# Optimization experiments

Measured on AMD Instinct MI355X. Metric: run time of the kernel, lower is better.

Reference implementation:

```python
import jax, jax.numpy as jnp
from jax import lax
import numpy as np

EPS_BN = 1e-5


def _convT(x, w, b, s, p):
    # PyTorch ConvTranspose2d(w: (Cin,Cout,k,k)) as gradient-of-conv.
    k = w.shape[2]
    wf = jnp.flip(w, (2, 3)).transpose(1, 0, 2, 3)  # (Cout,Cin,k,k)
    y = lax.conv_general_dilated(x, wf, (1, 1), [(k - 1 - p, k - 1 - p)] * 2,
                                 lhs_dilation=(s, s),
                                 dimension_numbers=('NCHW', 'OIHW', 'NCHW'))
    return y + b[None, :, None, None]


def _bn_relu(x, g, b):
    # BatchNorm2d in training mode (batch stats, biased var) + ReLU
    m = x.mean((0, 2, 3), keepdims=True)
    v = x.var((0, 2, 3), keepdims=True)
    return jax.nn.relu(g[None, :, None, None] * (x - m) * lax.rsqrt(v + EPS_BN) + b[None, :, None, None])


def _sn(w, u):
    # One power iteration (detached, as in the torch SpectralNorm impl), sigma through live w.
    wm = w.reshape(w.shape[0], -1)
    wd = lax.stop_gradient(wm)
    v = wd.T @ u
    v = v / (jnp.linalg.norm(v) + 1e-12)
    un = wd @ v
    un = un / (jnp.linalg.norm(un) + 1e-12)
    sigma = un @ (wm @ v)
    return w / sigma


def _self_attn(x, wf, bf, wg, bg, wh, bh, gamma):
    # Faithful math of Self_Attn, but without materializing the (b,C,N^2,N^2) repeat.
    b_, C, f, _ = x.shape
    N = f * f
    k = C // 8
    fx = (jnp.einsum('bchw,oc->bohw', x, wf) + bf[None, :, None, None]).reshape(b_, k, N, f, f)
    gx = (jnp.einsum('bchw,oc->bohw', x, wg) + bg[None, :, None, None]).reshape(b_, k, N, f, f)
    hx = (jnp.einsum('bchw,oc->bohw', x, wh) + bh[None, :, None, None]).reshape(b_, C, N)
    # attn_dist[b,i,a,c] = sum_k f_view[b,k,i,c,a] * g_view[b,k,i,a,c]  (f spatially transposed)
    logits = jnp.einsum('bkica,bkiac->biac', fx, gx).reshape(b_, N, N)
    attn = jax.nn.softmax(logits, axis=-1)  # (b, N, N)
    out = jnp.einsum('bcj,bij->bci', hx, attn).reshape(b_, C, f, f)
    return gamma[0] * out + x, attn[:, None]


def setup_inputs() -> dict:
    key = jax.random.key(0)
    ks = iter(jax.random.split(key, 64))

    def rn(shape, s=0.02):
        return jax.random.normal(next(ks), shape, jnp.float32) * s

    def uvec(n):
        u = jax.random.normal(next(ks), (n,), jnp.float32)
        return u / jnp.linalg.norm(u)

    B, Z = 4, 100
    d = {'z': jax.random.normal(next(ks), (B, Z), jnp.float32)}
    d.update(w1=rn((Z, 512, 4, 4)), b1=jnp.zeros(512), u1=uvec(Z), g1=jnp.ones(512), be1=jnp.zeros(512))
    d.update(w2=rn((512, 256, 4, 4)), b2=jnp.zeros(256), u2=uvec(512), g2=jnp.ones(256), be2=jnp.zeros(256))
    d.update(w3=rn((256, 128, 4, 4)), b3=jnp.zeros(128), u3=uvec(256), g3=jnp.ones(128), be3=jnp.zeros(128))
    d.update(w4=rn((128, 64, 4, 4)), b4=jnp.zeros(64), u4=uvec(128), g4=jnp.ones(64), be4=jnp.zeros(64))
    d.update(wl=rn((64, 3, 4, 4)), bl=jnp.zeros(3))
    d.update(wf1=rn((4096, 128)), bf1=jnp.zeros(4096), wg1=rn((4096, 128)), bg1=jnp.zeros(4096),
             wh1=rn((128, 128)), bh1=jnp.zeros(128), gamma1=jnp.full((1,), 0.5, jnp.float32))
    d.update(wf2=rn((8192, 64)), bf2=jnp.zeros(8192), wg2=rn((8192, 64)), bg2=jnp.zeros(8192),
             wh2=rn((64, 64)), bh2=jnp.zeros(64), gamma2=jnp.full((1,), 0.5, jnp.float32))
    return d


def reference(z, w1, b1, u1, g1, be1, w2, b2, u2, g2, be2, w3, b3, u3, g3, be3,
              w4, b4, u4, g4, be4, wl, bl,
              wf1, bf1, wg1, bg1, wh1, bh1, gamma1,
              wf2, bf2, wg2, bg2, wh2, bh2, gamma2):
    x = z[:, :, None, None]                                   # (B,100,1,1)
    x = _bn_relu(_convT(x, _sn(w1, u1), b1, 1, 0), g1, be1)   # (B,512,4,4)
    x = _bn_relu(_convT(x, _sn(w2, u2), b2, 2, 1), g2, be2)   # (B,256,8,8)
    x = _bn_relu(_convT(x, _sn(w3, u3), b3, 2, 1), g3, be3)   # (B,128,16,16)
    x, p1 = _self_attn(x, wf1, bf1, wg1, bg1, wh1, bh1, gamma1)
    x = _bn_relu(_convT(x, _sn(w4, u4), b4, 2, 1), g4, be4)   # (B,64,32,32)
    x, p2 = _self_attn(x, wf2, bf2, wg2, bg2, wh2, bh2, gamma2)
    out = jnp.tanh(_convT(x, wl, bl, 2, 1))                   # (B,3,64,64)
    return out, p1, p2
```

## Files before the change

kernel.cpp:

```cpp
#include <hip/hip_runtime.h>
#include <math.h>

#define DEV __device__ __forceinline__
typedef unsigned short ushort;
typedef __attribute__((ext_vector_type(8))) short bf16x8;
typedef __attribute__((ext_vector_type(4))) float f32x4;

constexpr int ACC   = 0;
constexpr int VR1   = 16;
constexpr int VR2   = VR1 + 8192;
constexpr int VR3   = VR2 + 4096;
constexpr int VR4   = VR3 + 2048;
constexpr int WS_Y1  = 16384;
constexpr int WS_Y2  = WS_Y1 + 32768;
constexpr int WS_Y3  = WS_Y2 + 65536;
constexpr int WS_BF3 = WS_Y3 + 131072;
constexpr int WS_H1T = WS_BF3 + 131072;
constexpr int WS_X3B = WS_H1T + 131072;
constexpr int WS_Y4  = WS_X3B + 131072;
constexpr int WS_BF4 = WS_Y4 + 262144;
constexpr int WS_H2T = WS_BF4 + 262144;
constexpr int WS_X4B = WS_H2T + 262144;
constexpr int WS_WB  = WS_X4B + 262144;
constexpr int WS_PART= WS_WB + 1048576;
constexpr int WS_WT2 = WS_PART + 1048576;
constexpr int WS_WT3 = WS_WT2 + 2097152;
constexpr int WS_WT4 = WS_WT3 + 524288;
constexpr int WS_WTL = WS_WT4 + 131072;

constexpr int O_P1 = 49152;
constexpr int O_P2 = O_P1 + 262144;

DEV ushort f2bf(float v){
  unsigned b = __float_as_uint(v);
  return (ushort)((b + 0x7fffu + ((b >> 16) & 1u)) >> 16);
}
DEV float wave_sum(float v){
  #pragma unroll
  for (int o = 32; o; o >>= 1) v += __shfl_xor(v, o, 64);
  return v;
}
DEV float wave_max(float v){
  #pragma unroll
  for (int o = 32; o; o >>= 1) v = fmaxf(v, __shfl_xor(v, o, 64));
  return v;
}
template<int T>
DEV float block_sum(float v, float* sm){
  v = wave_sum(v);
  if (T == 64) return v;
  __syncthreads();
  if ((threadIdx.x & 63) == 0) sm[threadIdx.x >> 6] = v;
  __syncthreads();
  float r = 0.f;
  #pragma unroll
  for (int i = 0; i < T/64; ++i) r += sm[i];
  return r;
}
template<int T>
DEV float block_max(float v, float* sm){
  v = wave_max(v);
  if (T == 64) return v;
  __syncthreads();
  if ((threadIdx.x & 63) == 0) sm[threadIdx.x >> 6] = v;
  __syncthreads();
  float r = -INFINITY;
  #pragma unroll
  for (int i = 0; i < T/64; ++i) r = fmaxf(r, sm[i]);
  return r;
}

DEV float inv_sigma(const float* __restrict__ ws, int wi){
  float d1 = sqrtf(ws[ACC + wi]) + 1e-12f;
  float s2 = ws[ACC + 4 + wi] / (d1 * d1);
  float sig = s2 / (sqrtf(s2) + 1e-12f);
  return 1.0f / sig;
}

__global__ void zero_vr_k(float* ws){
  int tid = blockIdx.x * 256 + threadIdx.x;
  ws[VR1 + tid] = 0.f;
  if (blockIdx.x == 0 && threadIdx.x < 8) ws[ACC + threadIdx.x] = 0.f;
}

__global__ void sn1_k(const float* __restrict__ w1, const float* __restrict__ w2,
                      const float* __restrict__ w3, const float* __restrict__ w4,
                      const float* __restrict__ u1, const float* __restrict__ u2,
                      const float* __restrict__ u3, const float* __restrict__ u4,
                      float* __restrict__ ws){
  int gid = blockIdx.x * 256 + threadIdx.x;
  int col_g = gid % 15360;
  int rchunk = gid / 15360;
  const float* W; const float* U; int rows, cols, col, voff;
  if (col_g < 8192)       { W=w1; U=u1; rows=100; cols=8192; col=col_g;        voff=VR1; }
  else if (col_g < 12288) { W=w2; U=u2; rows=512; cols=4096; col=col_g-8192;   voff=VR2; }
  else if (col_g < 14336) { W=w3; U=u3; rows=256; cols=2048; col=col_g-12288;  voff=VR3; }
  else                    { W=w4; U=u4; rows=128; cols=1024; col=col_g-14336;  voff=VR4; }
  int rc = rows >> 2;
  int r0 = rchunk * rc, r1 = r0 + rc;
  float a0=0.f, a1=0.f, a2=0.f, a3=0.f;
  int i = r0;
  for (; i + 3 < r1; i += 4){
    a0 = fmaf(W[(i  )*cols + col], U[i  ], a0);
    a1 = fmaf(W[(i+1)*cols + col], U[i+1], a1);
    a2 = fmaf(W[(i+2)*cols + col], U[i+2], a2);
    a3 = fmaf(W[(i+3)*cols + col], U[i+3], a3);
  }
  for (; i < r1; ++i) a0 = fmaf(W[i*cols + col], U[i], a0);
  atomicAdd(&ws[voff + col], (a0+a1)+(a2+a3));
}

__global__ void s1red_k(float* __restrict__ ws){
  int gid = blockIdx.x * 256 + threadIdx.x;
  int wi = gid < 8192 ? 0 : gid < 12288 ? 1 : gid < 14336 ? 2 : 3;
  float v = ws[VR1 + gid];
  float sq = wave_sum(v * v);
  if ((threadIdx.x & 63) == 0) atomicAdd(&ws[ACC + wi], sq);
}

__global__ void sn2_k(const float* __restrict__ w1, const float* __restrict__ w2,
                      const float* __restrict__ w3, const float* __restrict__ w4,
                      float* __restrict__ ws){
  int wave = (blockIdx.x * 256 + threadIdx.x) >> 6;
  int lane = threadIdx.x & 63;
  if (wave >= 996) return;
  const float* W; int row, cols, wi, voff;
  if (wave < 100)      { W=w1; row=wave;     cols=8192; wi=0; voff=VR1; }
  else if (wave < 612) { W=w2; row=wave-100; cols=4096; wi=1; voff=VR2; }
  else if (wave < 868) { W=w3; row=wave-612; cols=2048; wi=2; voff=VR3; }
  else                 { W=w4; row=wave-868; cols=1024; wi=3; voff=VR4; }
  const float* Wr = W + (size_t)row * cols;
  const float* Vr = ws + voff;
  float p0=0.f, p1=0.f, p2=0.f, p3=0.f;
  for (int j = lane; j < cols; j += 256){
    p0 = fmaf(Wr[j      ], Vr[j      ], p0);
    p1 = fmaf(Wr[j +  64], Vr[j +  64], p1);
    p2 = fmaf(Wr[j + 128], Vr[j + 128], p2);
    p3 = fmaf(Wr[j + 192], Vr[j + 192], p3);
  }
  float t = wave_sum((p0+p1)+(p2+p3));
  if (lane == 0) atomicAdd(&ws[ACC + 4 + wi], t * t);
}

__global__ void wtrans_k(const float* __restrict__ w2, const float* __restrict__ w3,
                         const float* __restrict__ w4, const float* __restrict__ wl,
                         const float* __restrict__ ws,
                         float* __restrict__ wt2, float* __restrict__ wt3,
                         float* __restrict__ wt4, float* __restrict__ wtl){
  int t = blockIdx.x * 256 + threadIdx.x;
  const float* src; float* dst; int CI, CO, loc; float inv;
  if (t < 2097152)      { src=w2; dst=wt2; CI=512; CO=256; loc=t;         inv=inv_sigma(ws,1); }
  else if (t < 2621440) { src=w3; dst=wt3; CI=256; CO=128; loc=t-2097152; inv=inv_sigma(ws,2); }
  else if (t < 2752512) { src=w4; dst=wt4; CI=128; CO=64;  loc=t-2621440; inv=inv_sigma(ws,3); }
  else                  { src=wl; dst=wtl; CI=64;  CO=3;   loc=t-2752512; inv=1.f; }
  int e  = loc & 3;
  int q  = loc >> 2;
  int co = q % CO;
  int ci = (q / CO) % CI;
  int p  = q / (CO * CI);
  int kh = (1 - (p >> 1)) + 2 * (e >> 1);
  int kw = (1 - (p & 1))  + 2 * (e & 1);
  dst[loc] = src[(ci*CO + co)*16 + kh*4 + kw] * inv;
}

__global__ void cvt_w_k(const float* __restrict__ a0, const float* __restrict__ a1,
                        const float* __restrict__ a2, const float* __restrict__ a3,
                        ushort* __restrict__ dst){
  int tid = blockIdx.x * 256 + threadIdx.x;
  int seg = tid >> 19;
  int off = tid & 524287;
  const float* s = seg == 0 ? a0 : seg == 1 ? a1 : seg == 2 ? a2 : a3;
  dst[tid] = f2bf(s[off]);
}

__global__ void conv1_k(const float* __restrict__ z, const float* __restrict__ w,
                        const float* __restrict__ bias, const float* __restrict__ ws,
                        float* __restrict__ y){
  int tid = blockIdx.x * 256 + threadIdx.x;
  int s  = tid & 15;
  int co = (tid >> 4) & 511;
  int b  = tid >> 13;
  float inv = inv_sigma(ws, 0);
  const float* zb = z + b*100;
  const float* wp = w + co*16 + s;
  float a0=0.f, a1=0.f, a2=0.f, a3=0.f;
  for (int ci = 0; ci < 100; ci += 4){
    a0 = fmaf(zb[ci  ], wp[(ci  )*8192], a0);
    a1 = fmaf(zb[ci+1], wp[(ci+1)*8192], a1);
    a2 = fmaf(zb[ci+2], wp[(ci+2)*8192], a2);
    a3 = fmaf(zb[ci+3], wp[(ci+3)*8192], a3);
  }
  y[tid] = ((a0+a1)+(a2+a3)) * inv + bias[co];
}

template<int CI, int CO, int IH>
__global__ __launch_bounds__(256) void convt_par_k(const float* __restrict__ x,
                                                   const float* __restrict__ wt,
                                                   float* __restrict__ partial){
  constexpr int OH   = 2 * IH;
  constexpr int TPJ  = 4 * IH * IH;
  constexpr int CIS  = CI / 4;
  constexpr int OUTS = 4 * CO * OH * OH;
  int tid = blockIdx.x * 256 + threadIdx.x;
  int within = tid % TPJ;
  int job    = tid / TPJ;
  int co = job % CO;
  int p  = (job / CO) & 3;
  int sc = job / (CO * 4);
  co = __builtin_amdgcn_readfirstlane(co);
  p  = __builtin_amdgcn_readfirstlane(p);
  sc = __builtin_amdgcn_readfirstlane(sc);
  int b  = within / (IH * IH);
  int rc = within % (IH * IH);
  int r = rc / IH, c = rc % IH;
  int po = p >> 1, pw = p & 1;
  int ih0 = r + po, ih1 = ih0 - 1;
  int iw0 = c + pw, iw1 = iw0 - 1;
  bool vh0 = ih0 < IH, vh1 = ih1 >= 0;
  bool vw0 = iw0 < IH, vw1 = iw1 >= 0;
  int jh0 = vh0 ? ih0 : 0, jh1 = vh1 ? ih1 : 0;
  int jw0 = vw0 ? iw0 : 0, jw1 = vw1 ? iw1 : 0;
  int o00 = jh0*IH + jw0, o01 = jh0*IH + jw1;
  int o10 = jh1*IH + jw0, o11 = jh1*IH + jw1;
  const float* xb = x + (b*CI + sc*CIS) * IH * IH;
  const float* wp = wt + (size_t)((p*CI + sc*CIS)*CO + co) * 4;
  float a00=0.f, a01=0.f, a10=0.f, a11=0.f;
  #pragma unroll 4
  for (int ci = 0; ci < CIS; ++ci){
    f32x4 wv = *(const f32x4*)(wp + (size_t)ci*CO*4);
    const float* xp = xb + ci*IH*IH;
    a00 = fmaf(xp[o00], wv[0], a00);
    a01 = fmaf(xp[o01], wv[1], a01);
    a10 = fmaf(xp[o10], wv[2], a10);
    a11 = fmaf(xp[o11], wv[3], a11);
  }
  float res = (vh0 && vw0 ? a00 : 0.f) + (vh0 && vw1 ? a01 : 0.f)
            + (vh1 && vw0 ? a10 : 0.f) + (vh1 && vw1 ? a11 : 0.f);
  int oh = 2*r + po, ow = 2*c + pw;
  partial[(size_t)sc*OUTS + ((b*CO + co)*OH + oh)*OH + ow] = res;
}

__global__ void tanh_comb_k(const float* __restrict__ partial,
                            const float* __restrict__ bl, float* __restrict__ out){
  int tid = blockIdx.x * 256 + threadIdx.x;
  int co = (tid >> 12) % 3;
  float a = partial[tid] + partial[49152 + tid] + partial[2*49152 + tid]
          + partial[3*49152 + tid] + bl[co];
  out[tid] = tanhf(a);
}

template<int C, int HW, int EPT, int THREADS>
__global__ void bn_relu_k(float* __restrict__ y, const float* __restrict__ g,
                          const float* __restrict__ be){
  __shared__ float sm[8];
  int c = blockIdx.x;
  int t = threadIdx.x;
  constexpr int N = 4 * HW;
  float v[EPT];
  #pragma unroll
  for (int k = 0; k < EPT; ++k){
    int e = t + k * THREADS;
    int b = e / HW, hw = e % HW;
    v[k] = y[(b*C + c)*HW + hw];
  }
  float s = 0.f;
  #pragma unroll
  for (int k = 0; k < EPT; ++k) s += v[k];
  s = block_sum<THREADS>(s, sm);
  float m = s / (float)N;
  float q = 0.f;
  #pragma unroll
  for (int k = 0; k < EPT; ++k){ float d = v[k] - m; q = fmaf(d, d, q); }
  q = block_sum<THREADS>(q, sm);
  float rstd = rsqrtf(q / (float)N + 1e-5f);
  float gg = g[c] * rstd, bb = be[c];
  #pragma unroll
  for (int k = 0; k < EPT; ++k){
    int e = t + k * THREADS;
    int b = e / HW, hw = e % HW;
    y[(b*C + c)*HW + hw] = fmaxf(fmaf(v[k] - m, gg, bb), 0.f);
  }
}

template<int C, int HW, int EPT, int THREADS>
__global__ void bn_relu_sum_k(const float* __restrict__ partial,
                              const float* __restrict__ bias,
                              const float* __restrict__ g, const float* __restrict__ be,
                              float* __restrict__ y){
  __shared__ float sm[8];
  constexpr int OUTS = 4 * C * HW;
  int c = blockIdx.x;
  int t = threadIdx.x;
  constexpr int N = 4 * HW;
  float cb = bias[c];
  float v[EPT];
  #pragma unroll
  for (int k = 0; k < EPT; ++k){
    int e = t + k * THREADS;
    int b = e / HW, hw = e % HW;
    int idx = (b*C + c)*HW + hw;
    v[k] = partial[idx] + partial[OUTS + idx] + partial[2*OUTS + idx]
         + partial[3*OUTS + idx] + cb;
  }
  float s = 0.f;
  #pragma unroll
  for (int k = 0; k < EPT; ++k) s += v[k];
  s = block_sum<THREADS>(s, sm);
  float m = s / (float)N;
  float q = 0.f;
  #pragma unroll
  for (int k = 0; k < EPT; ++k){ float d = v[k] - m; q = fmaf(d, d, q); }
  q = block_sum<THREADS>(q, sm);
  float rstd = rsqrtf(q / (float)N + 1e-5f);
  float gg = g[c] * rstd, bb = be[c];
  #pragma unroll
  for (int k = 0; k < EPT; ++k){
    int e = t + k * THREADS;
    int b = e / HW, hw = e % HW;
    y[(b*C + c)*HW + hw] = fmaxf(fmaf(v[k] - m, gg, bb), 0.f);
  }
}

template<int C, int F>
__global__ void prep_attn_k(const float* __restrict__ x, const float* __restrict__ wh,
                            const float* __restrict__ bh,
                            ushort* __restrict__ xs, ushort* __restrict__ xts,
                            ushort* __restrict__ hb){
  constexpr int N = F * F;
  constexpr int G1 = (4 * C * N) / 256;
  int blk = blockIdx.x;
  if (blk < G1){
    int tid = blk * 256 + threadIdx.x;
    int c = tid % C;
    int s = (tid / C) % N;
    int b = tid / (C * N);
    xs[tid]  = f2bf(x[(b*C + c)*N + s]);
    int ts = (s % F) * F + s / F;
    xts[tid] = f2bf(x[(b*C + c)*N + ts]);
  } else {
    int tid = (blk - G1) * 256 + threadIdx.x;
    int j  = tid % N;
    int cc = (tid / N) % C;
    int b  = tid / (N*C);
    float a = bh[cc];
    for (int ch = 0; ch < C; ++ch)
      a = fmaf(wh[cc*C + ch], x[(b*C + ch)*N + j], a);
    hb[tid] = f2bf(a);
  }
}

template<int C, int N, int K, int JPB>
__global__ __launch_bounds__(256) void logits_mfma_res_k(
    const ushort* __restrict__ xs, const ushort* __restrict__ xts,
    const ushort* __restrict__ wfb, const ushort* __restrict__ wgb,
    const float* __restrict__ bfp, const float* __restrict__ bgp,
    float* __restrict__ out){
  constexpr int NF  = C / 32;
  constexpr int NIG = N / 64;
  constexpr int NJC = (N / 16) / JPB;
  int w = threadIdx.x >> 6, l = threadIdx.x & 63;
  int lr = l & 15, lg = l >> 4;
  int blk = blockIdx.x;
  int jc = blk % NJC;
  int ib = (blk / NJC) % NIG;
  int b  = blk / (NJC * NIG);
  int i0 = ib * 64 + w * 16;
  int j0 = jc * (JPB * 16);

  bf16x8 af[K][NF], ag[K][NF];
  f32x4 bfv[K], bgv[K];
  #pragma unroll
  for (int kk = 0; kk < K; ++kk){
    #pragma unroll
    for (int f = 0; f < NF; ++f){
      int ro = (kk*N + i0 + lr)*C + f*32 + lg*8;
      af[kk][f] = *(const bf16x8*)(wfb + ro);
      ag[kk][f] = *(const bf16x8*)(wgb + ro);
    }
    bfv[kk] = *(const f32x4*)(bfp + kk*N + i0 + lg*4);
    bgv[kk] = *(const f32x4*)(bgp + kk*N + i0 + lg*4);
  }
  const ushort* xsp  = xs  + (b*N + j0 + lr)*C + lg*8;
  const ushort* xtsp = xts + (b*N + j0 + lr)*C + lg*8;
  float* op = out + (size_t)(b*N + i0 + lg*4)*N + j0 + lr;
  for (int it = 0; it < JPB; ++it){
    bf16x8 bs[NF], bt[NF];
    #pragma unroll
    for (int f = 0; f < NF; ++f){
      bs[f] = *(const bf16x8*)(xsp  + it*16*C + f*32);
      bt[f] = *(const bf16x8*)(xtsp + it*16*C + f*32);
    }
    f32x4 acc = {0.f, 0.f, 0.f, 0.f};
    #pragma unroll
    for (int kk = 0; kk < K; ++kk){
      f32x4 F = bfv[kk], G = bgv[kk];
      #pragma unroll
      for (int f = 0; f < NF; ++f){
        F = __builtin_amdgcn_mfma_f32_16x16x32_bf16(af[kk][f], bt[f], F, 0, 0, 0);
        G = __builtin_amdgcn_mfma_f32_16x16x32_bf16(ag[kk][f], bs[f], G, 0, 0, 0);
      }
      #pragma unroll
      for (int r = 0; r < 4; ++r) acc[r] = fmaf(F[r], G[r], acc[r]);
    }
    #pragma unroll
    for (int r = 0; r < 4; ++r) op[(size_t)r*N + it*16] = acc[r];
  }
}

template<int C, int N, int K, int JPB>
__global__ __launch_bounds__(256) void logits_mfma_split_k(
    const ushort* __restrict__ xs, const ushort* __restrict__ xts,
    const ushort* __restrict__ wfb, const ushort* __restrict__ wgb,
    const float* __restrict__ bfp, const float* __restrict__ bgp,
    float* __restrict__ out){
  constexpr int NF  = C / 32;
  constexpr int KW  = K / 4;
  constexpr int NJC = (N / 16) / JPB;
  __shared__ float red[3][320];
  int w = threadIdx.x >> 6, l = threadIdx.x & 63;
  int lr = l & 15, lg = l >> 4;
  int blk = blockIdx.x;
  int jc = blk % NJC;
  int ig = (blk / NJC) % (N / 16);
  int b  = blk / (NJC * (N / 16));
  int i0 = ig * 16;
  int j0 = jc * (JPB * 16);
  int k0 = w * KW;

  bf16x8 af[KW][NF], ag[KW][NF];
  f32x4 bfv[KW], bgv[KW];
  #pragma unroll
  for (int kk = 0; kk < KW; ++kk){
    #pragma unroll
    for (int f = 0; f < NF; ++f){
      int ro = ((k0 + kk)*N + i0 + lr)*C + f*32 + lg*8;
      af[kk][f] = *(const bf16x8*)(wfb + ro);
      ag[kk][f] = *(const bf16x8*)(wgb + ro);
    }
    bfv[kk] = *(const f32x4*)(bfp + (k0 + kk)*N + i0 + lg*4);
    bgv[kk] = *(const f32x4*)(bgp + (k0 + kk)*N + i0 + lg*4);
  }
  const ushort* xsp  = xs  + (b*N + j0 + lr)*C + lg*8;
  const ushort* xtsp = xts + (b*N + j0 + lr)*C + lg*8;
  float* op = out + (size_t)(b*N + i0 + lg*4)*N + j0 + lr;
  for (int it = 0; it < JPB; ++it){
    bf16x8 bs[NF], bt[NF];
    #pragma unroll
    for (int f = 0; f < NF; ++f){
      bs[f] = *(const bf16x8*)(xsp  + it*16*C + f*32);
      bt[f] = *(const bf16x8*)(xtsp + it*16*C + f*32);
    }
    f32x4 acc = {0.f, 0.f, 0.f, 0.f};
    #pragma unroll
    for (int kk = 0; kk < KW; ++kk){
      f32x4 F = bfv[kk], G = bgv[kk];
      #pragma unroll
      for (int f = 0; f < NF; ++f){
        F = __builtin_amdgcn_mfma_f32_16x16x32_bf16(af[kk][f], bt[f], F, 0, 0, 0);
        G = __builtin_amdgcn_mfma_f32_16x16x32_bf16(ag[kk][f], bs[f], G, 0, 0, 0);
      }
      #pragma unroll
      for (int r = 0; r < 4; ++r) acc[r] = fmaf(F[r], G[r], acc[r]);
    }
    if (w > 0){
      #pragma unroll
      for (int r = 0; r < 4; ++r) red[w-1][l*5 + r] = acc[r];
    }
    __syncthreads();
    if (w == 0){
      #pragma unroll
      for (int ww = 0; ww < 3; ++ww)
        #pragma unroll
        for (int r = 0; r < 4; ++r) acc[r] += red[ww][l*5 + r];
      #pragma unroll
      for (int r = 0; r < 4; ++r) op[(size_t)r*N + it*16] = acc[r];
    }
    __syncthreads();
  }
}

template<int LEN, int EPT>
__global__ void softmax_k(float* __restrict__ p, ushort* __restrict__ pb){
  __shared__ float sm[8];
  int row = blockIdx.x;
  int t = threadIdx.x;
  float v[EPT];
  #pragma unroll
  for (int k = 0; k < EPT; ++k) v[k] = p[row*LEN + t + k*256];
  float m = -INFINITY;
  #pragma unroll
  for (int k = 0; k < EPT; ++k) m = fmaxf(m, v[k]);
  m = block_max<256>(m, sm);
  float s = 0.f;
  #pragma unroll
  for (int k = 0; k < EPT; ++k){ v[k] = expf(v[k] - m); s += v[k]; }
  s = block_sum<256>(s, sm);
  #pragma unroll
  for (int k = 0; k < EPT; ++k){
    float r = v[k] / s;
    p[row*LEN + t + k*256]  = r;
    pb[row*LEN + t + k*256] = f2bf(r);
  }
}

template<int C, int N, int KS>
__global__ __launch_bounds__(256) void attnout_mfma_k(
    const ushort* __restrict__ pb, const ushort* __restrict__ hb,
    float* __restrict__ partial){
  constexpr int NIT = N / 16;
  constexpr int NCT = C / 16;
  constexpr int KC  = N / KS;
  constexpr int NKF = KC / 32;
  constexpr int SZ  = 4 * C * N;
  int w = threadIdx.x >> 6, l = threadIdx.x & 63;
  int lr = l & 15, lg = l >> 4;
  int wid = blockIdx.x * 4 + w;
  int ks  = wid % KS;
  int cct = (wid / KS) % NCT;
  int it  = (wid / (KS * NCT)) % NIT;
  int b   = wid / (KS * NCT * NIT);
  int koff = ks * KC;

  const ushort* pp = pb + (size_t)(b*N + it*16 + lr)*N + koff + lg*8;
  bf16x8 bfr[NKF];
  #pragma unroll
  for (int f = 0; f < NKF; ++f) bfr[f] = *(const bf16x8*)(pp + f*32);
  const ushort* hp = hb + (size_t)(b*C + cct*16 + lr)*N + koff + lg*8;
  f32x4 acc = {0.f, 0.f, 0.f, 0.f};
  #pragma unroll
  for (int f = 0; f < NKF; ++f){
    bf16x8 afr = *(const bf16x8*)(hp + f*32);
    acc = __builtin_amdgcn_mfma_f32_16x16x32_bf16(afr, bfr[f], acc, 0, 0, 0);
  }
  float* op = partial + (size_t)ks*SZ + ((size_t)(b*C + cct*16 + lg*4)*N + it*16 + lr);
  #pragma unroll
  for (int r = 0; r < 4; ++r) op[(size_t)r*N] = acc[r];
}

template<int C, int N, int KS>
__global__ void attnout_fin_k(const float* __restrict__ partial,
                              const float* __restrict__ x,
                              const float* __restrict__ gamma,
                              float* __restrict__ xo){
  constexpr int SZ = 4 * C * N;
  int tid = blockIdx.x * 256 + threadIdx.x;
  float s = 0.f;
  #pragma unroll
  for (int ks = 0; ks < KS; ++ks) s += partial[(size_t)ks*SZ + tid];
  xo[tid] = fmaf(gamma[0], s, x[tid]);
}

extern "C" void kernel_launch(void* const* d_in, const int* in_sizes, int n_in,
                              void* d_out, int out_size, void* d_ws, size_t ws_size,
                              hipStream_t stream){
  const float* z   = (const float*)d_in[0];
  const float* w1  = (const float*)d_in[1];  const float* b1  = (const float*)d_in[2];
  const float* u1  = (const float*)d_in[3];  const float* g1  = (const float*)d_in[4];
  const float* be1 = (const float*)d_in[5];
  const float* w2  = (const float*)d_in[6];  const float* b2  = (const float*)d_in[7];
  const float* u2  = (const float*)d_in[8];  const float* g2  = (const float*)d_in[9];
  const float* be2 = (const float*)d_in[10];
  const float* w3  = (const float*)d_in[11]; const float* b3  = (const float*)d_in[12];
  const float* u3  = (const float*)d_in[13]; const float* g3  = (const float*)d_in[14];
  const float* be3 = (const float*)d_in[15];
  const float* w4  = (const float*)d_in[16]; const float* b4  = (const float*)d_in[17];
  const float* u4  = (const float*)d_in[18]; const float* g4  = (const float*)d_in[19];
  const float* be4 = (const float*)d_in[20];
  const float* wl  = (const float*)d_in[21]; const float* bl  = (const float*)d_in[22];
  const float* wf1 = (const float*)d_in[23]; const float* bf1 = (const float*)d_in[24];
  const float* wg1 = (const float*)d_in[25]; const float* bg1 = (const float*)d_in[26];
  const float* wh1 = (const float*)d_in[27]; const float* bh1 = (const float*)d_in[28];
  const float* gamma1 = (const float*)d_in[29];
  const float* wf2 = (const float*)d_in[30]; const float* bf2 = (const float*)d_in[31];
  const float* wg2 = (const float*)d_in[32]; const float* bg2 = (const float*)d_in[33];
  const float* wh2 = (const float*)d_in[34]; const float* bh2 = (const float*)d_in[35];
  const float* gamma2 = (const float*)d_in[36];

  float* ws  = (float*)d_ws;
  float* out = (float*)d_out;

  ushort* wb    = (ushort*)(ws + WS_WB);
  ushort* wf1b  = wb;
  ushort* wg1b  = wb + 524288;
  ushort* wf2b  = wb + 2*524288;
  ushort* wg2b  = wb + 3*524288;
  ushort* xs3   = (ushort*)(ws + WS_BF3);
  ushort* xts3  = xs3 + 131072;
  ushort* xs4   = (ushort*)(ws + WS_BF4);
  ushort* xts4  = xs4 + 262144;
  ushort* hb1   = (ushort*)(ws + WS_H1T);
  ushort* hb2   = (ushort*)(ws + WS_H2T);
  ushort* pbuf  = (ushort*)(ws + WS_WT2);
  float*  part  = ws + WS_PART;

  zero_vr_k<<<60, 256, 0, stream>>>(ws);
  sn1_k<<<240, 256, 0, stream>>>(w1, w2, w3, w4, u1, u2, u3, u4, ws);
  s1red_k<<<60, 256, 0, stream>>>(ws);
  sn2_k<<<249, 256, 0, stream>>>(w1, w2, w3, w4, ws);
  wtrans_k<<<10764, 256, 0, stream>>>(w2, w3, w4, wl, ws,
                                      ws + WS_WT2, ws + WS_WT3, ws + WS_WT4, ws + WS_WTL);
  cvt_w_k<<<8192, 256, 0, stream>>>(wf1, wg1, wf2, wg2, wb);

  conv1_k<<<128, 256, 0, stream>>>(z, w1, b1, ws, ws + WS_Y1);
  bn_relu_k<512, 16, 1, 64><<<512, 64, 0, stream>>>(ws + WS_Y1, g1, be1);

  convt_par_k<512, 256, 4><<<1024, 256, 0, stream>>>(ws + WS_Y1, ws + WS_WT2, part);
  bn_relu_sum_k<256, 64, 1, 256><<<256, 256, 0, stream>>>(part, b2, g2, be2, ws + WS_Y2);

  convt_par_k<256, 128, 8><<<2048, 256, 0, stream>>>(ws + WS_Y2, ws + WS_WT3, part);
  bn_relu_sum_k<128, 256, 4, 256><<<128, 256, 0, stream>>>(part, b3, g3, be3, ws + WS_Y3);

  prep_attn_k<128, 16><<<1024, 256, 0, stream>>>(ws + WS_Y3, wh1, bh1, xs3, xts3, hb1);
  logits_mfma_split_k<128, 256, 16, 4><<<256, 256, 0, stream>>>(
      xs3, xts3, wf1b, wg1b, bf1, bg1, out + O_P1);
  softmax_k<256, 1><<<1024, 256, 0, stream>>>(out + O_P1, pbuf);
  attnout_mfma_k<128, 256, 1><<<128, 256, 0, stream>>>(pbuf, hb1, part);
  attnout_fin_k<128, 256, 1><<<512, 256, 0, stream>>>(part, ws + WS_Y3, gamma1,
                                                      ws + WS_X3B);

  convt_par_k<128, 64, 16><<<4096, 256, 0, stream>>>(ws + WS_X3B, ws + WS_WT4, part);
  bn_relu_sum_k<64, 1024, 16, 256><<<64, 256, 0, stream>>>(part, b4, g4, be4, ws + WS_Y4);

  prep_attn_k<64, 32><<<2048, 256, 0, stream>>>(ws + WS_Y4, wh2, bh2, xs4, xts4, hb2);
  logits_mfma_res_k<64, 1024, 8, 8><<<512, 256, 0, stream>>>(
      xs4, xts4, wf2b, wg2b, bf2, bg2, out + O_P2);
  softmax_k<1024, 4><<<4096, 256, 0, stream>>>(out + O_P2, pbuf);
  attnout_mfma_k<64, 1024, 4><<<1024, 256, 0, stream>>>(pbuf, hb2, part);
  attnout_fin_k<64, 1024, 4><<<1024, 256, 0, stream>>>(part, ws + WS_Y4, gamma2,
                                                       ws + WS_X4B);

  convt_par_k<64, 3, 32><<<768, 256, 0, stream>>>(ws + WS_X4B, ws + WS_WTL, part);
  tanh_comb_k<<<192, 256, 0, stream>>>(part, bl, out);
}
```

Measured before the change: 373.3 us.

## Fuse weight prep kernels, vectorize stores, widen BN and attention-output splits

Merges the weight transpose and bf16 conversion into one launch. Each thread now reads 16 contiguous taps and writes four f32x4 vectors, and the conversion uses 4-wide loads and stores. It also unrolls the h-projection with four accumulators and raises the first attention-output split from 1 to 2. The layer-4 BN kernel moves to 1024 threads per channel, which is why the shared reduction buffer grows to 16 entries. These changes target launch overhead and uncoalesced scalar memory traffic, at the cost of more code paths and a dependence on the larger reduction buffer.

```diff
diff --git a/kernel.cpp b/kernel.cpp
--- a/kernel.cpp
+++ b/kernel.cpp
@@ -5,6 +5,7 @@
 typedef unsigned short ushort;
 typedef __attribute__((ext_vector_type(8))) short bf16x8;
 typedef __attribute__((ext_vector_type(4))) float f32x4;
+typedef __attribute__((ext_vector_type(4))) ushort us4;
 
 constexpr int ACC   = 0;
 constexpr int VR1   = 16;
@@ -142,35 +143,51 @@
   if (lane == 0) atomicAdd(&ws[ACC + 4 + wi], t * t);
 }
 
-__global__ void wtrans_k(const float* __restrict__ w2, const float* __restrict__ w3,
-                         const float* __restrict__ w4, const float* __restrict__ wl,
-                         const float* __restrict__ ws,
-                         float* __restrict__ wt2, float* __restrict__ wt3,
-                         float* __restrict__ wt4, float* __restrict__ wtl){
-  int t = blockIdx.x * 256 + threadIdx.x;
-  const float* src; float* dst; int CI, CO, loc; float inv;
-  if (t < 2097152)      { src=w2; dst=wt2; CI=512; CO=256; loc=t;         inv=inv_sigma(ws,1); }
-  else if (t < 2621440) { src=w3; dst=wt3; CI=256; CO=128; loc=t-2097152; inv=inv_sigma(ws,2); }
-  else if (t < 2752512) { src=w4; dst=wt4; CI=128; CO=64;  loc=t-2621440; inv=inv_sigma(ws,3); }
-  else                  { src=wl; dst=wtl; CI=64;  CO=3;   loc=t-2752512; inv=1.f; }
-  int e  = loc & 3;
-  int q  = loc >> 2;
-  int co = q % CO;
-  int ci = (q / CO) % CI;
-  int p  = q / (CO * CI);
-  int kh = (1 - (p >> 1)) + 2 * (e >> 1);
-  int kw = (1 - (p & 1))  + 2 * (e & 1);
-  dst[loc] = src[(ci*CO + co)*16 + kh*4 + kw] * inv;
-}
-
-__global__ void cvt_w_k(const float* __restrict__ a0, const float* __restrict__ a1,
-                        const float* __restrict__ a2, const float* __restrict__ a3,
-                        ushort* __restrict__ dst){
-  int tid = blockIdx.x * 256 + threadIdx.x;
-  int seg = tid >> 19;
-  int off = tid & 524287;
-  const float* s = seg == 0 ? a0 : seg == 1 ? a1 : seg == 2 ? a2 : a3;
-  dst[tid] = f2bf(s[off]);
+__global__ void wprep_k(const float* __restrict__ w2, const float* __restrict__ w3,
+                        const float* __restrict__ w4, const float* __restrict__ wl,
+                        const float* __restrict__ ws,
+                        float* __restrict__ wt2, float* __restrict__ wt3,
+                        float* __restrict__ wt4, float* __restrict__ wtl,
+                        const float* __restrict__ wf1, const float* __restrict__ wg1,
+                        const float* __restrict__ wf2, const float* __restrict__ wg2,
+                        ushort* __restrict__ wbdst){
+  int blk = blockIdx.x;
+  if (blk < 673){
+    int t = blk * 256 + threadIdx.x;
+    if (t >= 172224) return;
+    const float* src; float* dst; int CI, CO, loc; float inv;
+    if (t < 131072)      { src=w2; dst=wt2; CI=512; CO=256; loc=t;        inv=inv_sigma(ws,1); }
+    else if (t < 163840) { src=w3; dst=wt3; CI=256; CO=128; loc=t-131072; inv=inv_sigma(ws,2); }
+    else if (t < 172032) { src=w4; dst=wt4; CI=128; CO=64;  loc=t-163840; inv=inv_sigma(ws,3); }
+    else                 { src=wl; dst=wtl; CI=64;  CO=3;   loc=t-172032; inv=1.f; }
+    int co = loc % CO, ci = loc / CO;
+    float wv[16];
+    const float* sp = src + (size_t)(ci*CO + co) * 16;
+    #pragma unroll
+    for (int k = 0; k < 16; ++k) wv[k] = sp[k] * inv;
+    #pragma unroll
+    for (int p = 0; p < 4; ++p){
+      int po = p >> 1, pw = p & 1;
+      f32x4 o;
+      #pragma unroll
+      for (int e = 0; e < 4; ++e){
+        int kh = (1 - po) + 2 * (e >> 1);
+        int kw = (1 - pw) + 2 * (e & 1);
+        o[e] = wv[kh*4 + kw];
+      }
+      *(f32x4*)(dst + (size_t)((p*CI + ci)*CO + co) * 4) = o;
+    }
+  } else {
+    int tid = (blk - 673) * 256 + threadIdx.x;
+    int seg = tid >> 17;
+    int off = (tid & 131071) * 4;
+    const float* s = seg == 0 ? wf1 : seg == 1 ? wg1 : seg == 2 ? wf2 : wg2;
+    f32x4 v = *(const f32x4*)(s + off);
+    us4 o;
+    #pragma unroll
+    for (int k = 0; k < 4; ++k) o[k] = f2bf(v[k]);
+    *(us4*)(wbdst + (size_t)seg*524288 + off) = o;
+  }
 }
 
 __global__ void conv1_k(const float* __restrict__ z, const float* __restrict__ w,
@@ -252,7 +269,7 @@
 template<int C, int HW, int EPT, int THREADS>
 __global__ void bn_relu_k(float* __restrict__ y, const float* __restrict__ g,
                           const float* __restrict__ be){
-  __shared__ float sm[8];
+  __shared__ float sm[16];
   int c = blockIdx.x;
   int t = threadIdx.x;
   constexpr int N = 4 * HW;
@@ -287,7 +304,7 @@
                               const float* __restrict__ bias,
                               const float* __restrict__ g, const float* __restrict__ be,
                               float* __restrict__ y){
-  __shared__ float sm[8];
+  __shared__ float sm[16];
   constexpr int OUTS = 4 * C * HW;
   int c = blockIdx.x;
   int t = threadIdx.x;
@@ -342,10 +359,17 @@
     int j  = tid % N;
     int cc = (tid / N) % C;
     int b  = tid / (N*C);
-    float a = bh[cc];
-    for (int ch = 0; ch < C; ++ch)
-      a = fmaf(wh[cc*C + ch], x[(b*C + ch)*N + j], a);
-    hb[tid] = f2bf(a);
+    const float* whp = wh + cc*C;
+    const float* xp  = x + (size_t)b*C*N + j;
+    float a0 = bh[cc], a1 = 0.f, a2 = 0.f, a3 = 0.f;
+    #pragma unroll 4
+    for (int ch = 0; ch < C; ch += 4){
+      a0 = fmaf(whp[ch  ], xp[(size_t)(ch  )*N], a0);
+      a1 = fmaf(whp[ch+1], xp[(size_t)(ch+1)*N], a1);
+      a2 = fmaf(whp[ch+2], xp[(size_t)(ch+2)*N], a2);
+      a3 = fmaf(whp[ch+3], xp[(size_t)(ch+3)*N], a3);
+    }
+    hb[tid] = f2bf((a0+a1)+(a2+a3));
   }
 }
 
@@ -481,7 +505,7 @@
 
 template<int LEN, int EPT>
 __global__ void softmax_k(float* __restrict__ p, ushort* __restrict__ pb){
-  __shared__ float sm[8];
+  __shared__ float sm[16];
   int row = blockIdx.x;
   int t = threadIdx.x;
   float v[EPT];
@@ -597,9 +621,9 @@
   sn1_k<<<240, 256, 0, stream>>>(w1, w2, w3, w4, u1, u2, u3, u4, ws);
   s1red_k<<<60, 256, 0, stream>>>(ws);
   sn2_k<<<249, 256, 0, stream>>>(w1, w2, w3, w4, ws);
-  wtrans_k<<<10764, 256, 0, stream>>>(w2, w3, w4, wl, ws,
-                                      ws + WS_WT2, ws + WS_WT3, ws + WS_WT4, ws + WS_WTL);
-  cvt_w_k<<<8192, 256, 0, stream>>>(wf1, wg1, wf2, wg2, wb);
+  wprep_k<<<2721, 256, 0, stream>>>(w2, w3, w4, wl, ws,
+                                    ws + WS_WT2, ws + WS_WT3, ws + WS_WT4, ws + WS_WTL,
+                                    wf1, wg1, wf2, wg2, wb);
 
   conv1_k<<<128, 256, 0, stream>>>(z, w1, b1, ws, ws + WS_Y1);
   bn_relu_k<512, 16, 1, 64><<<512, 64, 0, stream>>>(ws + WS_Y1, g1, be1);
@@ -614,12 +638,12 @@
   logits_mfma_split_k<128, 256, 16, 4><<<256, 256, 0, stream>>>(
       xs3, xts3, wf1b, wg1b, bf1, bg1, out + O_P1);
   softmax_k<256, 1><<<1024, 256, 0, stream>>>(out + O_P1, pbuf);
-  attnout_mfma_k<128, 256, 1><<<128, 256, 0, stream>>>(pbuf, hb1, part);
-  attnout_fin_k<128, 256, 1><<<512, 256, 0, stream>>>(part, ws + WS_Y3, gamma1,
+  attnout_mfma_k<128, 256, 2><<<256, 256, 0, stream>>>(pbuf, hb1, part);
+  attnout_fin_k<128, 256, 2><<<512, 256, 0, stream>>>(part, ws + WS_Y3, gamma1,
                                                       ws + WS_X3B);
 
   convt_par_k<128, 64, 16><<<4096, 256, 0, stream>>>(ws + WS_X3B, ws + WS_WT4, part);
-  bn_relu_sum_k<64, 1024, 16, 256><<<64, 256, 0, stream>>>(part, b4, g4, be4, ws + WS_Y4);
+  bn_relu_sum_k<64, 1024, 4, 1024><<<64, 1024, 0, stream>>>(part, b4, g4, be4, ws + WS_Y4);
 
   prep_attn_k<64, 32><<<2048, 256, 0, stream>>>(ws + WS_Y4, wh2, bh2, xs4, xts4, hb2);
   logits_mfma_res_k<64, 1024, 8, 8><<<512, 256, 0, stream>>>(
```

After: 361.9 us. 3.1% less time.
